# Optimization experiments

Hardware: AMD Instinct MI355X
Metric: run time of the kernel (lower is better)

## Reference

```python
import jax, jax.numpy as jnp
import numpy as np

N, E, C, NB = 10000, 160000, 32, 8  # atoms, edges, channels, radial basis


def _W(k, shp):
    return jax.random.normal(k, shp, jnp.float32) / np.float32(np.sqrt(shp[0]))


def setup_inputs():
    ks = jax.random.split(jax.random.key(0), 16)
    return {
        "p1": jax.random.normal(ks[0], (N, C), jnp.float32),
        "p3": jax.random.normal(ks[1], (N, 3, C), jnp.float32),
        "r3": jax.random.normal(ks[2], (E, 3), jnp.float32),
        "basis": jax.random.normal(ks[3], (E, NB), jnp.float32),
        "idx_i": jax.random.randint(ks[4], (E,), 0, N, jnp.int32),
        "idx_j": jax.random.randint(ks[5], (E,), 0, N, jnp.int32),
        "pp1_W": _W(ks[6], (C, C)), "pp1_b": jnp.zeros((C,), jnp.float32),
        "pi1_W1": _W(ks[7], (2 * C, C)), "pi1_b1": jnp.zeros((C,), jnp.float32),
        "pi1_W2": _W(ks[8], (C, 3 * C)), "pi1_b2": jnp.zeros((3 * C,), jnp.float32),
        "pi1_W3": _W(ks[9], (3 * C, 3 * C * NB)),
        "ii1_W": _W(ks[10], (C, C)), "ii1_b": jnp.zeros((C,), jnp.float32),
        "pp3_W": _W(ks[11], (C, C)), "pp3_b": jnp.zeros((C,), jnp.float32),
        "pi3_W1": _W(ks[12], (2 * C, C)), "pi3_b1": jnp.zeros((C,), jnp.float32),
        "pi3_W2": _W(ks[13], (C, C)), "pi3_b2": jnp.zeros((C,), jnp.float32),
        "pi3_W3": _W(ks[14], (C, C * NB)),
        "ii3_W": _W(ks[15], (C, C)), "ii3_b": jnp.zeros((C,), jnp.float32),
    }


def _pi_layer(prop, idx_i, idx_j, basis, W1, b1, W2, b2, W3, out_c):
    # gather both endpoints, concat, linear MLP (no activation, no last bias),
    # contract trailing basis axis with per-edge basis functions
    inter = jnp.concatenate([prop[idx_i], prop[idx_j]], axis=-1)  # [E, ..., 2C]
    h = inter @ W1 + b1
    h = h @ W2 + b2
    h = h @ W3                                   # [E, ..., out_c*NB]
    h = h.reshape(h.shape[:-1] + (out_c, NB))
    return jnp.einsum('e...cb,eb->e...c', h, basis)


def _forward(p1, p3, r3, basis, idx_i, idx_j,
             pp1_W, pp1_b, pi1_W1, pi1_b1, pi1_W2, pi1_b2, pi1_W3, ii1_W, ii1_b,
             pp3_W, pp3_b, pi3_W1, pi3_b1, pi3_W2, pi3_b2, pi3_W3, ii3_W, ii3_b):
    act = jnp.tanh
    # rank-1 branch
    p1h = act(p1 @ pp1_W + pp1_b)                                   # [N, C]
    i1 = _pi_layer(p1h, idx_i, idx_j, basis,
                   pi1_W1, pi1_b1, pi1_W2, pi1_b2, pi1_W3, 3 * C)   # [E, 3C]
    i1_1, i1_2, i1_3 = jnp.split(i1, 3, axis=-1)
    i1a = act(i1_1 @ ii1_W + ii1_b)                                  # [E, C]
    p1n = jax.ops.segment_sum(i1a, idx_j, num_segments=N)            # [N, C]
    # rank-3 (vector) branch
    p3h = act(p3 @ pp3_W + pp3_b)                                    # [N, 3, C]
    i3 = _pi_layer(p3h, idx_i, idx_j, basis,
                   pi3_W1, pi3_b1, pi3_W2, pi3_b2, pi3_W3, C)        # [E, 3, C]
    i3 = act(i3 @ ii3_W + ii3_b)
    # equivariant scale/add: i3*i1_2 + r3*i1_3 (broadcast over Cartesian axis)
    i3 = i3 * i1_2[:, None, :] + r3[:, :, None] * i1_3[:, None, :]   # [E, 3, C]
    p3n = jax.ops.segment_sum(i3, idx_j, num_segments=N)             # [N, 3, C]
    # dot layer + residual into p1, then rescale p3 by p1
    p1o = jnp.sum(p3n * p3n, axis=1) + p1n                           # [N, C]
    p3o = p3n * p1o[:, None, :]                                      # [N, 3, C]
    return p1o, p3o


def reference(p1, p3, r3, basis, idx_i, idx_j,
              pp1_W, pp1_b, pi1_W1, pi1_b1, pi1_W2, pi1_b2, pi1_W3, ii1_W, ii1_b,
              pp3_W, pp3_b, pi3_W1, pi3_b1, pi3_W2, pi3_b2, pi3_W3, ii3_W, ii3_b):
    return _forward(p1, p3, r3, basis, idx_i, idx_j,
                    pp1_W, pp1_b, pi1_W1, pi1_b1, pi1_W2, pi1_b2, pi1_W3, ii1_W, ii1_b,
                    pp3_W, pp3_b, pi3_W1, pi3_b1, pi3_W2, pi3_b2, pi3_W3, ii3_W, ii3_b)
```

## Files before the change

kernel.cpp:

```cpp
#include <hip/hip_runtime.h>
#include <math.h>

#define NN 10000
#define NE 160000

typedef __attribute__((ext_vector_type(8))) short s8v;
typedef __attribute__((ext_vector_type(4))) float f4v;
typedef unsigned short u16;

#define OFF_P1HB 0u
#define OFF_P3HB 640000u
#define OFF_WB   2560000u
#define OFF_SCR  2703360u
#define OFF_P1N  2736640u
#define OFF_P3N  4016640u

#define OWF1  0
#define OBB1  49152
#define OII1T 52224
#define OWF3  53248
#define OBB3  69632
#define OII3T 70656
#define NWB   71680

__device__ __forceinline__ short f2b(float f) {
    unsigned u = __float_as_uint(f);
    u += 0x7fffu + ((u >> 16) & 1u);
    return (short)(u >> 16);
}
__device__ __forceinline__ float tanhf_fast(float x) {
    float xc = fminf(9.f, fmaxf(-9.f, x));
    float e = __expf(2.f * xc);
    return (e - 1.f) * __builtin_amdgcn_rcpf(e + 1.f);
}

__global__ __launch_bounds__(256) void node_prep(
    const float* __restrict__ p1, const float* __restrict__ p3,
    const float* __restrict__ pp1_W, const float* __restrict__ pp1_b,
    const float* __restrict__ pp3_W, const float* __restrict__ pp3_b,
    u16* __restrict__ p1hb, u16* __restrict__ p3hb)
{
    __shared__ float Ws[2][32 * 32];
    __shared__ float bsm[2][32];
    int tid = threadIdx.x;
    for (int i = tid; i < 32 * 32; i += 256) { Ws[0][i] = pp1_W[i]; Ws[1][i] = pp3_W[i]; }
    if (tid < 32) { bsm[0][tid] = pp1_b[tid]; bsm[1][tid] = pp3_b[tid]; }
    __syncthreads();
    int idx = blockIdx.x * 256 + tid;
    int n = idx >> 7;
    int r = (idx >> 5) & 3;
    int c = idx & 31;
    int sel = (r == 0) ? 0 : 1;
    const float* in = (r == 0) ? (p1 + n * 32) : (p3 + (n * 3 + (r - 1)) * 32);
    float acc = bsm[sel][c];
    #pragma unroll
    for (int k = 0; k < 32; ++k) acc += in[k] * Ws[sel][k * 32 + c];
    short v = f2b(tanhf(acc));
    if (r == 0) p1hb[n * 32 + c] = (u16)v;
    else        p3hb[(n * 3 + (r - 1)) * 32 + c] = (u16)v;
}

__global__ __launch_bounds__(256) void wprep1(
    const float* __restrict__ W1, const float* __restrict__ W2,
    const float* __restrict__ b1, const float* __restrict__ b2,
    const float* __restrict__ W13, const float* __restrict__ W23,
    const float* __restrict__ b13, const float* __restrict__ b23,
    float* __restrict__ scr)
{
    float* T1  = scr;
    float* T3  = scr + 6144;
    float* bt1 = scr + 8192;
    float* bt3 = scr + 8288;
    int i = blockIdx.x * 256 + threadIdx.x;
    if (i < 6144) {
        int r = i / 96, c = i % 96;
        float a = 0.f;
        #pragma unroll 8
        for (int k = 0; k < 32; ++k) a += W1[r * 32 + k] * W2[k * 96 + c];
        T1[i] = a;
    } else if ((i -= 6144) < 2048) {
        int r = i / 32, c = i % 32;
        float a = 0.f;
        #pragma unroll 8
        for (int k = 0; k < 32; ++k) a += W13[r * 32 + k] * W23[k * 32 + c];
        T3[i] = a;
    } else if ((i -= 2048) < 96) {
        float a = b2[i];
        #pragma unroll 8
        for (int k = 0; k < 32; ++k) a += b1[k] * W2[k * 96 + i];
        bt1[i] = a;
    } else if ((i -= 96) < 32) {
        float a = b23[i];
        #pragma unroll 8
        for (int k = 0; k < 32; ++k) a += b13[k] * W23[k * 32 + i];
        bt3[i] = a;
    }
}

__global__ __launch_bounds__(256) void wprep2(
    const float* __restrict__ W3, const float* __restrict__ W33,
    const float* __restrict__ ii1, const float* __restrict__ ii3,
    const float* __restrict__ scr, u16* __restrict__ wb)
{
    const float* T1  = scr;
    const float* T3  = scr + 6144;
    const float* bt1 = scr + 8192;
    const float* bt3 = scr + 8288;
    int i0 = blockIdx.x * 256 + threadIdx.x;
    if (i0 >= NWB) return;
    int i = i0;
    float v = 0.f;
    if (i < 49152) {
        int b = i / 6144, r = i % 6144;
        int nt = r / 1024, r2 = r % 1024;
        int ks = r2 / 512, r3 = r2 & 511;
        int L = r3 >> 3, j = r3 & 7;
        int k = ks * 32 + (L >> 4) * 8 + j;
        int c = 16 * nt + (L & 15);
        float a = 0.f;
        #pragma unroll 8
        for (int q = 0; q < 96; ++q) a += T1[k * 96 + q] * W3[q * 768 + c * 8 + b];
        v = a;
    } else if ((i -= 49152) < 3072) {
        int nt = i / 512, r3 = i & 511;
        int L = r3 >> 3, j = r3 & 7;
        if ((L >> 4) == 0) {
            int x = (16 * nt + (L & 15)) * 8 + j;
            float a = 0.f;
            #pragma unroll 8
            for (int q = 0; q < 96; ++q) a += bt1[q] * W3[q * 768 + x];
            v = a;
        }
    } else if ((i -= 3072) < 1024) {
        int nt = i / 512, r3 = i & 511;
        int L = r3 >> 3, j = r3 & 7;
        v = ii1[((L >> 4) * 8 + j) * 32 + 16 * nt + (L & 15)];
    } else if ((i -= 1024) < 16384) {
        int b = i / 2048, r = i % 2048;
        int nt = r / 1024, r2 = r % 1024;
        int ks = r2 / 512, r3 = r2 & 511;
        int L = r3 >> 3, j = r3 & 7;
        int k = ks * 32 + (L >> 4) * 8 + j;
        int c = 16 * nt + (L & 15);
        float a = 0.f;
        #pragma unroll 8
        for (int q = 0; q < 32; ++q) a += T3[k * 32 + q] * W33[q * 256 + c * 8 + b];
        v = a;
    } else if ((i -= 16384) < 1024) {
        int nt = i / 512, r3 = i & 511;
        int L = r3 >> 3, j = r3 & 7;
        if ((L >> 4) == 0) {
            int x = (16 * nt + (L & 15)) * 8 + j;
            float a = 0.f;
            #pragma unroll 8
            for (int q = 0; q < 32; ++q) a += bt3[q] * W33[q * 256 + x];
            v = a;
        }
    } else {
        i -= 1024;
        int nt = i / 512, r3 = i & 511;
        int L = r3 >> 3, j = r3 & 7;
        v = ii3[((L >> 4) * 8 + j) * 32 + 16 * nt + (L & 15)];
    }
    wb[i0] = (u16)f2b(v);
}

__global__ __launch_bounds__(64, 3) void edge_kernel(
    const u16* __restrict__ p1hb, const u16* __restrict__ p3hb,
    const float* __restrict__ r3, const float* __restrict__ basis,
    const int* __restrict__ idx_i, const int* __restrict__ idx_j,
    const u16* __restrict__ wb,
    const float* __restrict__ ii1b, const float* __restrict__ ii3b,
    float* __restrict__ p1n, float* __restrict__ p3n)
{
    __shared__ int4 smem4[192];
    char* sw = (char*)smem4;
    int*   sIdxI = (int*)(sw + 0);
    int*   sIdxJ = (int*)(sw + 128);
    float* sBasT = (float*)(sw + 256);
    float* sR3   = (float*)(sw + 1280);
    u16*   sT2   = (u16*)(sw + 1664);

    const int l   = threadIdx.x & 63;
    const int r16 = l & 15;
    const int kg  = l >> 4;
    const int ebase = blockIdx.x * 32;

    if (l < 32) sIdxI[l] = idx_i[ebase + l];
    else        sIdxJ[l - 32] = idx_j[ebase + l - 32];
    {
        int e = l & 31, hf = l >> 5;
        const float4* bp = (const float4*)(basis + (size_t)(ebase + e) * 8);
        float4 q = bp[hf];
        sBasT[(4 * hf + 0) * 32 + e] = q.x;
        sBasT[(4 * hf + 1) * 32 + e] = q.y;
        sBasT[(4 * hf + 2) * 32 + e] = q.z;
        sBasT[(4 * hf + 3) * 32 + e] = q.w;
        if (hf == 0) {
            sR3[e]      = r3[(size_t)(ebase + e) * 3 + 0];
            sR3[32 + e] = r3[(size_t)(ebase + e) * 3 + 1];
            sR3[64 + e] = r3[(size_t)(ebase + e) * 3 + 2];
        }
    }

    const float vii1[2] = { ii1b[r16], ii1b[16 + r16] };
    const float vii3[2] = { ii3b[r16], ii3b[16 + r16] };

    const f4v zf = {0.f, 0.f, 0.f, 0.f};

    s8v bA[2];
    #pragma unroll
    for (int m = 0; m < 2; ++m) {
        s8v t;
        #pragma unroll
        for (int j = 0; j < 8; ++j)
            t[j] = (kg == 0) ? f2b(sBasT[j * 32 + m * 16 + r16]) : (short)0;
        bA[m] = t;
    }

    s8v avI[2], avJ[2];
    #pragma unroll
    for (int m = 0; m < 2; ++m) {
        int rowA = m * 16 + r16;
        avI[m] = *(const s8v*)(p1hb + (size_t)sIdxI[rowA] * 32 + kg * 8);
        avJ[m] = *(const s8v*)(p1hb + (size_t)sIdxJ[rowA] * 32 + kg * 8);
    }

    f4v accT[2][6];
    {
        const u16* gBB = wb + OBB1;
        #pragma unroll
        for (int nt = 0; nt < 6; ++nt) {
            s8v bbv = *(const s8v*)(gBB + (nt * 64 + l) * 8);
            #pragma unroll
            for (int m = 0; m < 2; ++m)
                accT[m][nt] = __builtin_amdgcn_mfma_f32_16x16x32_bf16(bA[m], bbv, zf, 0, 0, 0);
        }
    }

    {
        const u16* gW = wb + OWF1;
        #pragma unroll 2
        for (int b = 0; b < 8; ++b) {
            float tb[2][4];
            #pragma unroll
            for (int m = 0; m < 2; ++m)
                #pragma unroll
                for (int rr = 0; rr < 4; ++rr)
                    tb[m][rr] = sBasT[b * 32 + m * 16 + 4 * kg + rr];
            #pragma unroll
            for (int nt = 0; nt < 6; ++nt) {
                const u16* bp = gW + ((size_t)(b * 6 + nt) * 2) * 512 + l * 8;
                s8v bv0 = *(const s8v*)(bp);
                s8v bv1 = *(const s8v*)(bp + 512);
                #pragma unroll
                for (int m = 0; m < 2; ++m) {
                    f4v D = __builtin_amdgcn_mfma_f32_16x16x32_bf16(avI[m], bv0, zf, 0, 0, 0);
                    D = __builtin_amdgcn_mfma_f32_16x16x32_bf16(avJ[m], bv1, D, 0, 0, 0);
                    #pragma unroll
                    for (int rr = 0; rr < 4; ++rr)
                        accT[m][nt][rr] += tb[m][rr] * D[rr];
                }
            }
        }
    }

    {
        const u16* gII = wb + OII1T;
        #pragma unroll
        for (int m = 0; m < 2; ++m) {
            #pragma unroll
            for (int nt = 0; nt < 2; ++nt)
                #pragma unroll
                for (int rr = 0; rr < 4; ++rr)
                    sT2[(4 * kg + rr) * 40 + 16 * nt + r16] = (u16)f2b(accT[m][nt][rr]);
            s8v av = *(const s8v*)(sT2 + r16 * 40 + 8 * kg);
            #pragma unroll
            for (int nt = 0; nt < 2; ++nt) {
                s8v bv = *(const s8v*)(gII + (nt * 64 + l) * 8);
                f4v ia = __builtin_amdgcn_mfma_f32_16x16x32_bf16(av, bv, zf, 0, 0, 0);
                #pragma unroll
                for (int rr = 0; rr < 4; ++rr) {
                    int rowD = m * 16 + 4 * kg + rr;
                    atomicAdd(&p1n[(size_t)sIdxJ[rowD] * 32 + 16 * nt + r16],
                              tanhf_fast(ia[rr] + vii1[nt]));
                }
            }
        }
    }

    const u16* gW3  = wb + OWF3;
    const u16* gBB3 = wb + OBB3;
    const u16* gII3 = wb + OII3T;
    for (int d = 0; d < 3; ++d) {
        s8v avI3[2], avJ3[2];
        #pragma unroll
        for (int m = 0; m < 2; ++m) {
            int rowA = m * 16 + r16;
            avI3[m] = *(const s8v*)(p3hb + ((size_t)sIdxI[rowA] * 3 + d) * 32 + kg * 8);
            avJ3[m] = *(const s8v*)(p3hb + ((size_t)sIdxJ[rowA] * 3 + d) * 32 + kg * 8);
        }
        f4v accP[2][2];
        #pragma unroll
        for (int nt = 0; nt < 2; ++nt) {
            s8v bbv = *(const s8v*)(gBB3 + (nt * 64 + l) * 8);
            #pragma unroll
            for (int m = 0; m < 2; ++m)
                accP[m][nt] = __builtin_amdgcn_mfma_f32_16x16x32_bf16(bA[m], bbv, zf, 0, 0, 0);
        }
        #pragma unroll 2
        for (int b = 0; b < 8; ++b) {
            float tb[2][4];
            #pragma unroll
            for (int m = 0; m < 2; ++m)
                #pragma unroll
                for (int rr = 0; rr < 4; ++rr)
                    tb[m][rr] = sBasT[b * 32 + m * 16 + 4 * kg + rr];
            #pragma unroll
            for (int nt = 0; nt < 2; ++nt) {
                const u16* bp = gW3 + ((size_t)(b * 2 + nt) * 2) * 512 + l * 8;
                s8v bv0 = *(const s8v*)(bp);
                s8v bv1 = *(const s8v*)(bp + 512);
                #pragma unroll
                for (int m = 0; m < 2; ++m) {
                    f4v D = __builtin_amdgcn_mfma_f32_16x16x32_bf16(avI3[m], bv0, zf, 0, 0, 0);
                    D = __builtin_amdgcn_mfma_f32_16x16x32_bf16(avJ3[m], bv1, D, 0, 0, 0);
                    #pragma unroll
                    for (int rr = 0; rr < 4; ++rr)
                        accP[m][nt][rr] += tb[m][rr] * D[rr];
                }
            }
        }
        #pragma unroll
        for (int m = 0; m < 2; ++m) {
            #pragma unroll
            for (int nt = 0; nt < 2; ++nt)
                #pragma unroll
                for (int rr = 0; rr < 4; ++rr)
                    sT2[(4 * kg + rr) * 40 + 16 * nt + r16] = (u16)f2b(accP[m][nt][rr]);
            s8v av = *(const s8v*)(sT2 + r16 * 40 + 8 * kg);
            #pragma unroll
            for (int nt = 0; nt < 2; ++nt) {
                s8v bv = *(const s8v*)(gII3 + (nt * 64 + l) * 8);
                f4v ja = __builtin_amdgcn_mfma_f32_16x16x32_bf16(av, bv, zf, 0, 0, 0);
                #pragma unroll
                for (int rr = 0; rr < 4; ++rr) {
                    int rowD = m * 16 + 4 * kg + rr;
                    float i3a = tanhf_fast(ja[rr] + vii3[nt]);
                    float val = i3a * accT[m][2 + nt][rr] + sR3[d * 32 + rowD] * accT[m][4 + nt][rr];
                    atomicAdd(&p3n[((size_t)sIdxJ[rowD] * 3 + d) * 32 + 16 * nt + r16], val);
                }
            }
        }
    }
}

__global__ __launch_bounds__(256) void finalize_kernel(
    const float* __restrict__ p1n, const float* __restrict__ p3n,
    float* __restrict__ out)
{
    int t = blockIdx.x * 256 + threadIdx.x;
    int n = t >> 5, c = t & 31;
    float a0 = p3n[(n * 3 + 0) * 32 + c];
    float a1 = p3n[(n * 3 + 1) * 32 + c];
    float a2 = p3n[(n * 3 + 2) * 32 + c];
    float p1o = p1n[t] + a0 * a0 + a1 * a1 + a2 * a2;
    out[t] = p1o;
    float* o3 = out + NN * 32;
    o3[(n * 3 + 0) * 32 + c] = a0 * p1o;
    o3[(n * 3 + 1) * 32 + c] = a1 * p1o;
    o3[(n * 3 + 2) * 32 + c] = a2 * p1o;
}

extern "C" void kernel_launch(void* const* d_in, const int* in_sizes, int n_in,
                              void* d_out, int out_size, void* d_ws, size_t ws_size,
                              hipStream_t stream) {
    const float* p1     = (const float*)d_in[0];
    const float* p3     = (const float*)d_in[1];
    const float* r3     = (const float*)d_in[2];
    const float* basis  = (const float*)d_in[3];
    const int*   idx_i  = (const int*)d_in[4];
    const int*   idx_j  = (const int*)d_in[5];
    const float* pp1_W  = (const float*)d_in[6];
    const float* pp1_b  = (const float*)d_in[7];
    const float* pi1_W1 = (const float*)d_in[8];
    const float* pi1_b1 = (const float*)d_in[9];
    const float* pi1_W2 = (const float*)d_in[10];
    const float* pi1_b2 = (const float*)d_in[11];
    const float* pi1_W3 = (const float*)d_in[12];
    const float* ii1_W  = (const float*)d_in[13];
    const float* ii1_b  = (const float*)d_in[14];
    const float* pp3_W  = (const float*)d_in[15];
    const float* pp3_b  = (const float*)d_in[16];
    const float* pi3_W1 = (const float*)d_in[17];
    const float* pi3_b1 = (const float*)d_in[18];
    const float* pi3_W2 = (const float*)d_in[19];
    const float* pi3_b2 = (const float*)d_in[20];
    const float* pi3_W3 = (const float*)d_in[21];
    const float* ii3_W  = (const float*)d_in[22];
    const float* ii3_b  = (const float*)d_in[23];

    char* ws = (char*)d_ws;
    u16*   p1hb = (u16*)(ws + OFF_P1HB);
    u16*   p3hb = (u16*)(ws + OFF_P3HB);
    u16*   wb   = (u16*)(ws + OFF_WB);
    float* scr  = (float*)(ws + OFF_SCR);
    float* p1n  = (float*)(ws + OFF_P1N);
    float* p3n  = (float*)(ws + OFF_P3N);

    hipMemsetAsync(p1n, 0, 5120000, stream);

    node_prep<<<dim3(5000), dim3(256), 0, stream>>>(p1, p3, pp1_W, pp1_b, pp3_W, pp3_b, p1hb, p3hb);
    wprep1<<<dim3(33), dim3(256), 0, stream>>>(
        pi1_W1, pi1_W2, pi1_b1, pi1_b2, pi3_W1, pi3_W2, pi3_b1, pi3_b2, scr);
    wprep2<<<dim3(NWB / 256), dim3(256), 0, stream>>>(
        pi1_W3, pi3_W3, ii1_W, ii3_W, scr, wb);

    edge_kernel<<<dim3(NE / 32), dim3(64), 0, stream>>>(
        p1hb, p3hb, r3, basis, idx_i, idx_j, wb,
        ii1_b, ii3_b, p1n, p3n);

    finalize_kernel<<<dim3(1250), dim3(256), 0, stream>>>(p1n, p3n, (float*)d_out);
}
```

Measured before the change: 136.9 us.

## Stage weight-prep tables in LDS, prefetch p3 rows, split transpose buffers

wprep2 now copies its intermediate T1/T3/bias tables from global scratch into shared memory before computing the fused weights. In edge_kernel the p3 gathers for the next Cartesian component are issued one iteration ahead of their use. Each m/d step also gets its own sT2 transpose slice, which removes write-after-read hazards in LDS. The edge kernel's occupancy hint rises from 3 to 4 waves, which adds register pressure, and its LDS footprint grows. A grid-size rounding fix is included but has no effect because NWB is a multiple of 256.

```diff
diff --git a/kernel.cpp b/kernel.cpp
--- a/kernel.cpp
+++ b/kernel.cpp
@@ -102,11 +102,16 @@
     const float* __restrict__ ii1, const float* __restrict__ ii3,
     const float* __restrict__ scr, u16* __restrict__ wb)
 {
-    const float* T1  = scr;
-    const float* T3  = scr + 6144;
-    const float* bt1 = scr + 8192;
-    const float* bt3 = scr + 8288;
-    int i0 = blockIdx.x * 256 + threadIdx.x;
+    __shared__ float sT1[6144];
+    __shared__ float sT3[2048];
+    __shared__ float sbt[128];
+    int tid = threadIdx.x;
+    for (int i = tid; i < 6144; i += 256) sT1[i] = scr[i];
+    for (int i = tid; i < 2048; i += 256) sT3[i] = scr[6144 + i];
+    if (tid < 128) sbt[tid] = scr[8192 + tid];
+    __syncthreads();
+
+    int i0 = blockIdx.x * 256 + tid;
     if (i0 >= NWB) return;
     int i = i0;
     float v = 0.f;
@@ -119,7 +124,7 @@
         int c = 16 * nt + (L & 15);
         float a = 0.f;
         #pragma unroll 8
-        for (int q = 0; q < 96; ++q) a += T1[k * 96 + q] * W3[q * 768 + c * 8 + b];
+        for (int q = 0; q < 96; ++q) a += sT1[k * 96 + q] * W3[q * 768 + c * 8 + b];
         v = a;
     } else if ((i -= 49152) < 3072) {
         int nt = i / 512, r3 = i & 511;
@@ -128,7 +133,7 @@
             int x = (16 * nt + (L & 15)) * 8 + j;
             float a = 0.f;
             #pragma unroll 8
-            for (int q = 0; q < 96; ++q) a += bt1[q] * W3[q * 768 + x];
+            for (int q = 0; q < 96; ++q) a += sbt[q] * W3[q * 768 + x];
             v = a;
         }
     } else if ((i -= 3072) < 1024) {
@@ -144,7 +149,7 @@
         int c = 16 * nt + (L & 15);
         float a = 0.f;
         #pragma unroll 8
-        for (int q = 0; q < 32; ++q) a += T3[k * 32 + q] * W33[q * 256 + c * 8 + b];
+        for (int q = 0; q < 32; ++q) a += sT3[k * 32 + q] * W33[q * 256 + c * 8 + b];
         v = a;
     } else if ((i -= 16384) < 1024) {
         int nt = i / 512, r3 = i & 511;
@@ -153,7 +158,7 @@
             int x = (16 * nt + (L & 15)) * 8 + j;
             float a = 0.f;
             #pragma unroll 8
-            for (int q = 0; q < 32; ++q) a += bt3[q] * W33[q * 256 + x];
+            for (int q = 0; q < 32; ++q) a += sbt[96 + q] * W33[q * 256 + x];
             v = a;
         }
     } else {
@@ -165,7 +170,7 @@
     wb[i0] = (u16)f2b(v);
 }
 
-__global__ __launch_bounds__(64, 3) void edge_kernel(
+__global__ __launch_bounds__(64, 4) void edge_kernel(
     const u16* __restrict__ p1hb, const u16* __restrict__ p3hb,
     const float* __restrict__ r3, const float* __restrict__ basis,
     const int* __restrict__ idx_i, const int* __restrict__ idx_j,
@@ -173,7 +178,7 @@
     const float* __restrict__ ii1b, const float* __restrict__ ii3b,
     float* __restrict__ p1n, float* __restrict__ p3n)
 {
-    __shared__ int4 smem4[192];
+    __shared__ int4 smem4[744];
     char* sw = (char*)smem4;
     int*   sIdxI = (int*)(sw + 0);
     int*   sIdxJ = (int*)(sw + 128);
@@ -269,12 +274,13 @@
         const u16* gII = wb + OII1T;
         #pragma unroll
         for (int m = 0; m < 2; ++m) {
+            u16* T2 = sT2 + m * 640;
             #pragma unroll
             for (int nt = 0; nt < 2; ++nt)
                 #pragma unroll
                 for (int rr = 0; rr < 4; ++rr)
-                    sT2[(4 * kg + rr) * 40 + 16 * nt + r16] = (u16)f2b(accT[m][nt][rr]);
-            s8v av = *(const s8v*)(sT2 + r16 * 40 + 8 * kg);
+                    T2[(4 * kg + rr) * 40 + 16 * nt + r16] = (u16)f2b(accT[m][nt][rr]);
+            s8v av = *(const s8v*)(T2 + r16 * 40 + 8 * kg);
             #pragma unroll
             for (int nt = 0; nt < 2; ++nt) {
                 s8v bv = *(const s8v*)(gII + (nt * 64 + l) * 8);
@@ -292,13 +298,25 @@
     const u16* gW3  = wb + OWF3;
     const u16* gBB3 = wb + OBB3;
     const u16* gII3 = wb + OII3T;
+    s8v nI3[2], nJ3[2];
+    #pragma unroll
+    for (int m = 0; m < 2; ++m) {
+        int rowA = m * 16 + r16;
+        nI3[m] = *(const s8v*)(p3hb + ((size_t)sIdxI[rowA] * 3 + 0) * 32 + kg * 8);
+        nJ3[m] = *(const s8v*)(p3hb + ((size_t)sIdxJ[rowA] * 3 + 0) * 32 + kg * 8);
+    }
+    #pragma unroll 1
     for (int d = 0; d < 3; ++d) {
         s8v avI3[2], avJ3[2];
-        #pragma unroll
-        for (int m = 0; m < 2; ++m) {
-            int rowA = m * 16 + r16;
-            avI3[m] = *(const s8v*)(p3hb + ((size_t)sIdxI[rowA] * 3 + d) * 32 + kg * 8);
-            avJ3[m] = *(const s8v*)(p3hb + ((size_t)sIdxJ[rowA] * 3 + d) * 32 + kg * 8);
+        avI3[0] = nI3[0]; avI3[1] = nI3[1];
+        avJ3[0] = nJ3[0]; avJ3[1] = nJ3[1];
+        if (d < 2) {
+            #pragma unroll
+            for (int m = 0; m < 2; ++m) {
+                int rowA = m * 16 + r16;
+                nI3[m] = *(const s8v*)(p3hb + ((size_t)sIdxI[rowA] * 3 + d + 1) * 32 + kg * 8);
+                nJ3[m] = *(const s8v*)(p3hb + ((size_t)sIdxJ[rowA] * 3 + d + 1) * 32 + kg * 8);
+            }
         }
         f4v accP[2][2];
         #pragma unroll
@@ -333,12 +351,13 @@
         }
         #pragma unroll
         for (int m = 0; m < 2; ++m) {
+            u16* T2 = sT2 + (2 + d * 2 + m) * 640;
             #pragma unroll
             for (int nt = 0; nt < 2; ++nt)
                 #pragma unroll
                 for (int rr = 0; rr < 4; ++rr)
-                    sT2[(4 * kg + rr) * 40 + 16 * nt + r16] = (u16)f2b(accP[m][nt][rr]);
-            s8v av = *(const s8v*)(sT2 + r16 * 40 + 8 * kg);
+                    T2[(4 * kg + rr) * 40 + 16 * nt + r16] = (u16)f2b(accP[m][nt][rr]);
+            s8v av = *(const s8v*)(T2 + r16 * 40 + 8 * kg);
             #pragma unroll
             for (int nt = 0; nt < 2; ++nt) {
                 s8v bv = *(const s8v*)(gII3 + (nt * 64 + l) * 8);
@@ -413,7 +432,7 @@
     node_prep<<<dim3(5000), dim3(256), 0, stream>>>(p1, p3, pp1_W, pp1_b, pp3_W, pp3_b, p1hb, p3hb);
     wprep1<<<dim3(33), dim3(256), 0, stream>>>(
         pi1_W1, pi1_W2, pi1_b1, pi1_b2, pi3_W1, pi3_W2, pi3_b1, pi3_b2, scr);
-    wprep2<<<dim3(NWB / 256), dim3(256), 0, stream>>>(
+    wprep2<<<dim3((NWB + 255) / 256), dim3(256), 0, stream>>>(
         pi1_W3, pi3_W3, ii1_W, ii3_W, scr, wb);
 
     edge_kernel<<<dim3(NE / 32), dim3(64), 0, stream>>>(
```

After: 179.1 us. +30.8%, slower.
